# Kernel optimization log

Measured on AMD Instinct MI355X. Metric: run time of the kernel, lower is better.

Reference implementation:

```python
import jax, jax.numpy as jnp
import numpy as np

N_NODES = 2048
UNITS = 64
IN_DIM = 64
K_DIFF = 2  # max_diffusion_step


def _rw_norm_t(adj):
    # random-walk normalize D^{-1}(A+I), then transpose (as in forward())
    a = adj + jnp.eye(adj.shape[0], dtype=adj.dtype)
    d = jnp.sum(a, axis=1)
    d_inv = jnp.where(d > 0, 1.0 / jnp.where(d > 0, d, 1.0), 0.0)
    return (d_inv[:, None] * a).T


def _gconv(x_cat, adj_t, W, b):
    # x_cat: (B, N, F). Chebyshev-like diffusion: x0, A x0, 2 A x1 - x0, ...
    x0 = x_cat
    xs = [x0]
    x1 = jnp.einsum('nm,bmf->bnf', adj_t, x0)
    xs.append(x1)
    for _ in range(2, K_DIFF + 1):
        x2 = 2.0 * jnp.einsum('nm,bmf->bnf', adj_t, x1) - x0
        xs.append(x2)
        x0, x1 = x1, x2
    x = jnp.stack(xs, axis=-1)  # (B, N, F, K+1) -> matches torch permute(3,1,2,0)
    B, N, F, K = x.shape
    x = x.reshape(B * N, F * K)
    out = x @ W + b
    return out.reshape(B, N, -1)


def setup_inputs() -> dict:
    key = jax.random.key(0)
    ks = jax.random.split(key, 6)
    B = 64
    inputs = jax.random.normal(ks[0], (B, N_NODES * IN_DIM), dtype=jnp.float32)
    hx = jax.random.normal(ks[1], (B, N_NODES * UNITS), dtype=jnp.float32)
    adj = jax.random.uniform(ks[2], (N_NODES, N_NODES), dtype=jnp.float32)
    in_sz = IN_DIM + UNITS
    nm = K_DIFF + 1
    scale = float(np.sqrt(2.0 / (in_sz * nm + 2 * UNITS)))  # xavier-ish
    W_ru = jax.random.normal(ks[3], (in_sz * nm, 2 * UNITS), dtype=jnp.float32) * scale
    b_ru = jnp.ones((2 * UNITS,), dtype=jnp.float32)  # bias_start=1.0
    W_c = jax.random.normal(ks[4], (in_sz * nm, UNITS), dtype=jnp.float32) * scale
    b_c = jnp.zeros((UNITS,), dtype=jnp.float32)
    return {"inputs": inputs, "hx": hx, "adj": adj,
            "W_ru": W_ru, "b_ru": b_ru, "W_c": W_c, "b_c": b_c}


def reference(inputs, hx, adj, W_ru, b_ru, W_c, b_c):
    B = inputs.shape[0]
    x = inputs.reshape(B, N_NODES, IN_DIM)
    h = hx.reshape(B, N_NODES, UNITS)
    adj_t = _rw_norm_t(adj)
    # r/u gates via graph conv + sigmoid
    ru = jax.nn.sigmoid(_gconv(jnp.concatenate([x, h], axis=-1), adj_t, W_ru, b_ru))
    r, u = ru[..., :UNITS], ru[..., UNITS:]
    # candidate state
    c = jnp.tanh(_gconv(jnp.concatenate([x, r * h], axis=-1), adj_t, W_c, b_c))
    new_state = u * h + (1.0 - u) * c
    return new_state.reshape(B, N_NODES * UNITS)
```

## Files before the change

kernel.cpp:

```cpp
#include <hip/hip_runtime.h>
#include <math.h>

typedef __attribute__((ext_vector_type(8))) short short8;
typedef __attribute__((ext_vector_type(4))) float float4v;
typedef __attribute__((ext_vector_type(16))) float float16v;
typedef __attribute__((ext_vector_type(4))) unsigned short ushort4v;
typedef unsigned short u16;
typedef unsigned int u32;

#define NB 64
#define NN 2048
#define FD 128
#define UD 64
#define KT 384


__device__ __forceinline__ u16 f2bf(float f) {
    unsigned int u = __float_as_uint(f);
    u += 0x7fffu + ((u >> 16) & 1u);
    return (u16)(u >> 16);
}
__device__ __forceinline__ float bf2f(u16 s) {
    return __uint_as_float(((unsigned int)s) << 16);
}
__device__ __forceinline__ float sigmoidf_(float x) {
    return 1.0f / (1.0f + expf(-x));
}
__device__ __forceinline__ void gl2lds16(const u16* g, u16* l) {
    __builtin_amdgcn_global_load_lds((const __attribute__((address_space(1))) unsigned int*)g,
                                     (__attribute__((address_space(3))) unsigned int*)l,
                                     16, 0, 0);
}

__global__ void k_prep(const float* __restrict__ adj, float* __restrict__ d_inv,
                       const float* __restrict__ W_ru, u16* __restrict__ Wru,
                       const float* __restrict__ W_c,  u16* __restrict__ Wc,
                       const float* __restrict__ x, const float* __restrict__ h,
                       u16* __restrict__ X0f, u16* __restrict__ X0m) {
    __shared__ u16 T[128 * 136];
    int bid = blockIdx.x;
    int t = threadIdx.x;
    if (bid < 2048) {
        int m = bid;
        const float4v* row = (const float4v*)(adj + (size_t)m * NN);
        float s = 0.f;
        for (int i = t; i < NN / 4; i += 256) {
            float4v v = row[i];
            s += v.x + v.y + v.z + v.w;
        }
        float* red = (float*)T;
        for (int off = 32; off; off >>= 1) s += __shfl_down(s, off, 64);
        if ((t & 63) == 0) red[t >> 6] = s;
        __syncthreads();
        if (t == 0) {
            float tt = red[0] + red[1] + red[2] + red[3] + 1.0f;
            d_inv[m] = 1.0f / tt;
        }
        return;
    }
    if (bid < 2336) {
        const float* W; u16* Wt; int OD, idx;
        if (bid < 2240) { W = W_ru; Wt = Wru; OD = FD; idx = (bid - 2048) * 256 + t; }
        else            { W = W_c;  Wt = Wc;  OD = UD; idx = (bid - 2240) * 256 + t; }
        if (idx >= KT * OD) return;
        int o  = idx % OD;
        int kp = idx / OD;
        int kd = kp >> 7, f = kp & 127;
        float v;
        if (kd == 0)      v = W[(size_t)(f * 3 + 0) * OD + o] - W[(size_t)(f * 3 + 2) * OD + o];
        else if (kd == 1) v = W[(size_t)(f * 3 + 1) * OD + o];
        else              v = 2.0f * W[(size_t)(f * 3 + 2) * OD + o];
        size_t dst = ((size_t)(o >> 5) * 12 + (kp >> 5)) * 1024 + (((kp >> 3) & 3) * 32 + (o & 31)) * 8 + (kp & 7);
        Wt[dst] = f2bf(v);
        return;
    }
    int rb = bid - 2336;
    int m0 = (rb & 15) * 128;
    int b  = rb >> 4;
    const float* srcs[2] = { x + (size_t)b * (NN * 64), h + (size_t)b * (NN * 64) };
    for (int s = 0; s < 2; ++s) {
        const float* src = srcs[s];
        for (int p = 0; p < 8; ++p) {
            int idx = t + 256 * p;
            int mi = idx >> 4;
            int f4 = idx & 15;
            float4v v = *(const float4v*)(src + (size_t)(m0 + mi) * 64 + f4 * 4);
            float vv[4] = {v.x, v.y, v.z, v.w};
#pragma unroll
            for (int j = 0; j < 4; ++j)
                T[(s * 64 + f4 * 4 + j) * 136 + mi] = f2bf(vv[j]);
        }
    }
    __syncthreads();
#pragma unroll
    for (int p = 0; p < 8; ++p) {
        int S = t + 256 * p;
        int fgl = S >> 9, kgl = (S >> 7) & 3, s = S & 127;
        int c = s >> 5, r = s & 31;
        short8 v = *(const short8*)(T + (fgl * 32 + r) * 136 + kgl * 32 + c * 8);
        *(short8*)(X0f + ((size_t)(b * 4 + fgl) * 64 + (m0 >> 5) + kgl) * 1024 + s * 8) = v;
    }
#pragma unroll
    for (int p = 0; p < 8; ++p) {
        int S = t + 256 * p;
        int fc = S >> 7;
        int mi = S & 127;
        short8 v;
#pragma unroll
        for (int e = 0; e < 8; ++e) v[e] = (short)T[(fc * 8 + e) * 136 + mi];
        size_t dst = ((size_t)(b * 64 + (m0 >> 5) + (mi >> 5)) * 4 + (fc >> 2)) * 1024
                     + ((fc & 3) * 32 + (mi & 31)) * 8;
        *(short8*)(X0m + dst) = v;
    }
}

__global__ void k_adjT(const float* __restrict__ adj, const float* __restrict__ d_inv,
                       u16* __restrict__ adjT) {
    __shared__ u16 T[64 * 72];
    int m0 = blockIdx.x * 64;
    int n0 = blockIdx.y * 64;
    int t = threadIdx.x;
    for (int p = 0; p < 4; ++p) {
        int idx = t + 256 * p;
        int i  = idx >> 4;
        int n4 = idx & 15;
        int m = m0 + i;
        float4v v = *(const float4v*)(adj + (size_t)m * NN + n0 + n4 * 4);
        float di = d_inv[m];
        float vv[4] = {v.x, v.y, v.z, v.w};
#pragma unroll
        for (int j = 0; j < 4; ++j) {
            int n = n0 + n4 * 4 + j;
            float a = vv[j] + ((m == n) ? 1.0f : 0.0f);
            T[(n4 * 4 + j) * 72 + i] = f2bf(a * di);
        }
    }
    __syncthreads();
#pragma unroll
    for (int p = 0; p < 2; ++p) {
        int S = t + 256 * p;
        int rgl = S >> 8, kgl = (S >> 7) & 1, s = S & 127;
        int c = s >> 5, r = s & 31;
        short8 v = *(const short8*)(T + (rgl * 32 + r) * 72 + kgl * 32 + c * 8);
        *(short8*)(adjT + ((size_t)((n0 >> 5) + rgl) * 64 + (m0 >> 5) + kgl) * 1024 + s * 8) = v;
    }
}

template<int HAS_F>
__global__ __launch_bounds__(512, 2)
void k_gemm256(const u16* __restrict__ Ap, const u16* __restrict__ Bc,
               u16* __restrict__ outF, u16* __restrict__ outM) {
    __shared__ __align__(16) u16 SM[81920];
    int bid = blockIdx.x;
    int wxcd = bid >> 3;
    int cb = (bid & 7) * 4 + (wxcd & 3);
    int nb = wxcd >> 2;
    int n0 = nb * 256, c0 = cb * 256;
    int t = threadIdx.x;
    int wave = t >> 6, lane = t & 63;
    int wx = wave >> 2;
    int wy = wave & 3;
    int ln = lane & 31, hi = lane >> 5;

    const u16* gA[2];
    const u16* gB[2];
    int la[2], lb[2];
#pragma unroll
    for (int i = 0; i < 2; ++i) {
        int idx = i * 512 + t;
        int p = idx >> 7, s = idx & 127;
        gA[i] = Bc + ((size_t)((c0 >> 5) + p) * 64) * 1024 + s * 8;
        gB[i] = Ap + ((size_t)((n0 >> 5) + p) * 64) * 1024 + s * 8;
        la[i] = idx * 8;
        lb[i] = 8192 + idx * 8;
    }

    float16v acc[4][2];
#pragma unroll
    for (int mt = 0; mt < 4; ++mt)
#pragma unroll
        for (int nt = 0; nt < 2; ++nt)
#pragma unroll
            for (int e = 0; e < 16; ++e) acc[mt][nt][e] = 0.f;

#pragma unroll
    for (int tt = 0; tt < 4; ++tt) {
#pragma unroll
        for (int i = 0; i < 2; ++i) gl2lds16(gA[i] + tt * 1024, SM + tt * 16384 + la[i]);
#pragma unroll
        for (int i = 0; i < 2; ++i) gl2lds16(gB[i] + tt * 1024, SM + tt * 16384 + lb[i]);
    }
    asm volatile("s_waitcnt vmcnt(12)" ::: "memory");
    __builtin_amdgcn_s_barrier();
    __builtin_amdgcn_sched_barrier(0);

    int rdA = wx * 4096 + lane * 8;
    int rdB = 8192 + wy * 2048 + lane * 8;

    int cur = 0;
    for (int kt = 0; kt < 64; ++kt) {
        u16* buf = SM + cur * 16384;
        int stg = cur + 4; if (stg >= 5) stg -= 5;
        u16* sbuf = SM + stg * 16384;
        size_t ko = (size_t)(kt + 4) * 1024;

        short8 fa0[4], fb0[2], fa1[4], fb1[2];
#pragma unroll
        for (int mt = 0; mt < 4; ++mt) fa0[mt] = *(const short8*)(buf + rdA + mt * 1024);
#pragma unroll
        for (int nt = 0; nt < 2; ++nt) fb0[nt] = *(const short8*)(buf + rdB + nt * 1024);
        if (kt < 60) {
#pragma unroll
            for (int i = 0; i < 2; ++i) gl2lds16(gA[i] + ko, sbuf + la[i]);
        }
#pragma unroll
        for (int mt = 0; mt < 4; ++mt) fa1[mt] = *(const short8*)(buf + rdA + mt * 1024 + 512);

        __builtin_amdgcn_s_setprio(1);
#pragma unroll
        for (int mt = 0; mt < 4; ++mt)
#pragma unroll
            for (int nt = 0; nt < 2; ++nt)
                acc[mt][nt] = __builtin_amdgcn_mfma_f32_32x32x16_bf16(fa0[mt], fb0[nt], acc[mt][nt], 0, 0, 0);
        __builtin_amdgcn_s_setprio(0);

#pragma unroll
        for (int nt = 0; nt < 2; ++nt) fb1[nt] = *(const short8*)(buf + rdB + nt * 1024 + 512);
        if (kt < 60) {
#pragma unroll
            for (int i = 0; i < 2; ++i) gl2lds16(gB[i] + ko, sbuf + lb[i]);
        }

        __builtin_amdgcn_s_setprio(1);
#pragma unroll
        for (int mt = 0; mt < 4; ++mt)
#pragma unroll
            for (int nt = 0; nt < 2; ++nt)
                acc[mt][nt] = __builtin_amdgcn_mfma_f32_32x32x16_bf16(fa1[mt], fb1[nt], acc[mt][nt], 0, 0, 0);
        __builtin_amdgcn_s_setprio(0);

        if (kt < 60)       asm volatile("s_waitcnt vmcnt(12)" ::: "memory");
        else if (kt == 60) asm volatile("s_waitcnt vmcnt(8)"  ::: "memory");
        else if (kt == 61) asm volatile("s_waitcnt vmcnt(4)"  ::: "memory");
        else if (kt == 62) asm volatile("s_waitcnt vmcnt(0)"  ::: "memory");
        if (kt < 63) {
            __builtin_amdgcn_s_barrier();
            __builtin_amdgcn_sched_barrier(0);
        }
        cur = (cur + 1 == 5) ? 0 : cur + 1;
    }

    int batch0 = cb * 2 + wx;
#pragma unroll
    for (int mt = 0; mt < 4; ++mt) {
#pragma unroll
        for (int nt = 0; nt < 2; ++nt) {
            int mg = (n0 >> 5) + wy * 2 + nt;
            size_t pbase = ((size_t)(batch0 * 64 + mg) * 4 + mt) * 1024;
#pragma unroll
            for (int eq = 0; eq < 4; ++eq) {
                ushort4v pk;
#pragma unroll
                for (int r = 0; r < 4; ++r) pk[r] = f2bf(acc[mt][nt][eq * 4 + r]);
                *(ushort4v*)(outM + pbase + (eq * 32 + ln) * 8 + 4 * hi) = pk;
            }
        }
    }

    if (HAS_F) {
#pragma unroll
        for (int p = 0; p < 2; ++p) {
            __syncthreads();
            if ((wy >> 1) == p) {
#pragma unroll
                for (int mt = 0; mt < 4; ++mt)
#pragma unroll
                    for (int nt = 0; nt < 2; ++nt)
#pragma unroll
                        for (int e = 0; e < 16; ++e) {
                            int cl = wx * 128 + mt * 32 + 4 * hi + 8 * (e >> 2) + (e & 3);
                            int nl = (wy & 1) * 64 + nt * 32 + ln;
                            SM[cl * 136 + nl] = f2bf(acc[mt][nt][e]);
                        }
            }
            __syncthreads();
#pragma unroll
            for (int j = 0; j < 8; ++j) {
                int S = t + 512 * j;
                int col = S >> 4, nd8 = S & 15;
                short8 v = *(const short8*)(SM + col * 136 + nd8 * 8);
                int gn = n0 + p * 128 + nd8 * 8;
                size_t dst = ((size_t)((c0 >> 5) + (col >> 5)) * 64 + (gn >> 5)) * 1024
                             + (size_t)((((gn >> 3) & 3) * 32 + (col & 31))) * 8;
                *(short8*)(outF + dst) = v;
            }
        }
    }
}

template<int FG>
__global__ __launch_bounds__(256, 4)
void k_gemm(const u16* __restrict__ A, const u16* __restrict__ Bc,
            u16* __restrict__ outF, u16* __restrict__ outM, int cBlocks) {
    __shared__ u16 SM[16384];
    u16* A0 = SM;            u16* A1 = SM + 4096;
    u16* B0 = SM + 8192;     u16* B1 = SM + 12288;

    int id = blockIdx.x + cBlocks * blockIdx.y;
    int band = cBlocks >> 3;
    int g = id & 7, s = id >> 3;
    int cb = g * band + (s % band);
    int nb = s / band;
    int c0 = cb * 128;
    int n0 = nb * 128;

    int t = threadIdx.x;
    int wave = t >> 6, lane = t & 63;
    int wy = wave & 1, wx = wave >> 1;
    int ln = lane & 31, hi = lane >> 5;
    int l16 = lane * 8;

    const u16* gaP[2];
    const u16* gbP[2];
#pragma unroll
    for (int i = 0; i < 2; ++i) {
        int T = t + 256 * i;
        gaP[i] = A  + ((size_t)((n0 >> 5) + (T >> 7)) * 64) * 1024 + (size_t)(T & 127) * 8;
        gbP[i] = Bc + ((size_t)((c0 >> 5) + (T >> 7)) * 64) * 1024 + (size_t)(T & 127) * 8;
    }

    float16v acc[2][2];
#pragma unroll
    for (int i = 0; i < 2; ++i)
#pragma unroll
        for (int j = 0; j < 2; ++j)
#pragma unroll
            for (int e = 0; e < 16; ++e) acc[i][j][e] = 0.f;

#pragma unroll
    for (int i = 0; i < 2; ++i) { gl2lds16(gaP[i], A0 + (t + 256 * i) * 8); gl2lds16(gbP[i], B0 + (t + 256 * i) * 8); }

#pragma unroll 2
    for (int it = 0; it < 64; ++it) {
        u16* Ac = (it & 1) ? A1 : A0;
        u16* Bs = (it & 1) ? B1 : B0;
        __syncthreads();
        if (it + 1 < 64) {
            int ko = (it + 1) * 1024;
            u16* An = (it & 1) ? A0 : A1;
            u16* Bn = (it & 1) ? B0 : B1;
#pragma unroll
            for (int i = 0; i < 2; ++i) { gl2lds16(gaP[i] + ko, An + (t + 256 * i) * 8); gl2lds16(gbP[i] + ko, Bn + (t + 256 * i) * 8); }
        }
        short8 fa[2][2], fb[2][2];
#pragma unroll
        for (int ks = 0; ks < 2; ++ks) {
#pragma unroll
            for (int mt = 0; mt < 2; ++mt)
                fa[ks][mt] = *(const short8*)(Bs + ((wx * 2 + mt) * 2 + ks) * 512 + l16);
#pragma unroll
            for (int nt = 0; nt < 2; ++nt)
                fb[ks][nt] = *(const short8*)(Ac + ((wy * 2 + nt) * 2 + ks) * 512 + l16);
        }
#pragma unroll
        for (int ks = 0; ks < 2; ++ks)
#pragma unroll
            for (int mt = 0; mt < 2; ++mt)
#pragma unroll
                for (int nt = 0; nt < 2; ++nt)
                    acc[mt][nt] = __builtin_amdgcn_mfma_f32_32x32x16_bf16(fa[ks][mt], fb[ks][nt], acc[mt][nt], 0, 0, 0);
    }

#pragma unroll
    for (int mt = 0; mt < 2; ++mt) {
#pragma unroll
        for (int nt = 0; nt < 2; ++nt) {
            int mg = (n0 >> 5) + wy * 2 + nt;
            int batch = (FG == 4) ? cb : (2 * cb + wx);
            int fg = (FG == 4) ? (wx * 2 + mt) : mt;
            size_t pbase = ((size_t)(batch * 64 + mg) * FG + fg) * 1024;
#pragma unroll
            for (int eq = 0; eq < 4; ++eq) {
                ushort4v pk;
#pragma unroll
                for (int r = 0; r < 4; ++r) pk[r] = f2bf(acc[mt][nt][eq * 4 + r]);
                *(ushort4v*)(outM + pbase + (eq * 32 + ln) * 8 + 4 * hi) = pk;
            }
        }
    }

    if (outF) {
        __syncthreads();
#pragma unroll
        for (int p = 0; p < 2; ++p) {
            if (p) __syncthreads();
            if (wx == p) {
#pragma unroll
                for (int mt = 0; mt < 2; ++mt)
#pragma unroll
                    for (int nt = 0; nt < 2; ++nt)
#pragma unroll
                        for (int e = 0; e < 16; ++e) {
                            int cl = mt * 32 + 4 * hi + 8 * (e >> 2) + (e & 3);
                            int nl = wy * 64 + nt * 32 + ln;
                            SM[cl * 136 + nl] = f2bf(acc[mt][nt][e]);
                        }
            }
            __syncthreads();
#pragma unroll
            for (int pp = 0; pp < 4; ++pp) {
                int S = t + 256 * pp;
                int rgl = S >> 9, kgl = (S >> 7) & 3, sl = S & 127;
                int c = sl >> 5, r = sl & 31;
                short8 v = *(const short8*)(SM + (rgl * 32 + r) * 136 + kgl * 32 + c * 8);
                size_t gaddr = ((size_t)((c0 >> 5) + p * 2 + rgl) * 64 + (n0 >> 5) + kgl) * 1024 + sl * 8;
                *(short8*)(outF + gaddr) = v;
            }
        }
    }
}

__global__ __launch_bounds__(256, 3)
void k_proj_ru(const u16* __restrict__ X0m, const u16* __restrict__ X1m, const u16* __restrict__ Ym,
               const u16* __restrict__ Wp, const float* __restrict__ bias, const float* __restrict__ hx,
               u16* __restrict__ RH0f, u16* __restrict__ RH0m, u16* __restrict__ Ut) {
    __shared__ u16 SM[24576];
    int mb = blockIdx.x, b = blockIdx.y;
    int m0 = mb * 128, mg0 = mb * 4;
    int t = threadIdx.x, wave = t >> 6, lane = t & 63;
    int wx = wave & 1, wyy = wave >> 1;
    int ln = lane & 31, hi = lane >> 5;
    const u16* Xs[3] = {X0m, X1m, Ym};
    int p0 = t >> 7, s0 = t & 127;

    float16v acc[2][2];
#pragma unroll
    for (int i = 0; i < 2; ++i)
#pragma unroll
        for (int j = 0; j < 2; ++j)
#pragma unroll
            for (int e = 0; e < 16; ++e) acc[i][j][e] = 0.f;

#define STAGE_RU(Q, XD, WD) { \
    const u16* xb_ = Xs[(Q) >> 2]; \
    gl2lds16(xb_ + ((size_t)((b * 64 + mg0 + p0) * 4 + ((Q) & 3))) * 1024 + s0 * 8, (XD) + t * 8); \
    gl2lds16(xb_ + ((size_t)((b * 64 + mg0 + p0 + 2) * 4 + ((Q) & 3))) * 1024 + s0 * 8, (XD) + (t + 256) * 8); \
    gl2lds16(Wp + ((size_t)(p0 * 12 + (Q))) * 1024 + s0 * 8, (WD) + t * 8); \
    gl2lds16(Wp + ((size_t)((p0 + 2) * 12 + (Q))) * 1024 + s0 * 8, (WD) + (t + 256) * 8); }

    STAGE_RU(0, SM,        SM + 12288);
    STAGE_RU(1, SM + 4096, SM + 16384);
    asm volatile("s_waitcnt vmcnt(4)" ::: "memory");
    __builtin_amdgcn_s_barrier();
    __builtin_amdgcn_sched_barrier(0);

    int q0 = 0, q1 = 1, q2 = 2;
    for (int kq = 0; kq < 12; ++kq) {
        u16* Xc = SM + q0 * 4096;
        u16* Wc = SM + 12288 + q0 * 4096;
        if (kq + 2 < 12) STAGE_RU(kq + 2, SM + q2 * 4096, SM + 12288 + q2 * 4096);
        short8 fa[2][2], fb[2][2];
#pragma unroll
        for (int ks = 0; ks < 2; ++ks) {
#pragma unroll
            for (int mt = 0; mt < 2; ++mt)
                fa[ks][mt] = *(const short8*)(Xc + ((wx * 2 + mt) * 2 + ks) * 512 + lane * 8);
#pragma unroll
            for (int nt = 0; nt < 2; ++nt)
                fb[ks][nt] = *(const short8*)(Wc + ((wyy * 2 + nt) * 2 + ks) * 512 + lane * 8);
        }
        __builtin_amdgcn_s_setprio(1);
#pragma unroll
        for (int ks = 0; ks < 2; ++ks)
#pragma unroll
            for (int mt = 0; mt < 2; ++mt)
#pragma unroll
                for (int nt = 0; nt < 2; ++nt)
                    acc[mt][nt] = __builtin_amdgcn_mfma_f32_32x32x16_bf16(fa[ks][mt], fb[ks][nt], acc[mt][nt], 0, 0, 0);
        __builtin_amdgcn_s_setprio(0);
        if (kq < 10)       asm volatile("s_waitcnt vmcnt(4)" ::: "memory");
        else if (kq == 10) asm volatile("s_waitcnt vmcnt(0)" ::: "memory");
        if (kq < 11) {
            __builtin_amdgcn_s_barrier();
            __builtin_amdgcn_sched_barrier(0);
        }
        int tq = q0; q0 = q1; q1 = q2; q2 = tq;
    }
#undef STAGE_RU

    __syncthreads();
    if (wyy == 0) {
#pragma unroll
        for (int mt = 0; mt < 2; ++mt)
#pragma unroll
            for (int nt = 0; nt < 2; ++nt) {
                int o = nt * 32 + ln;
                float bo = bias[o];
                u16 vals[16];
#pragma unroll
                for (int e = 0; e < 16; ++e) {
                    int ml = wx * 64 + mt * 32 + 4 * hi + 8 * (e >> 2) + (e & 3);
                    float sg = sigmoidf_(acc[mt][nt][e] + bo);
                    float hh = hx[((size_t)b * NN + m0 + ml) * 64 + o];
                    vals[e] = f2bf(sg * hh);
                    SM[ml * 76 + o] = vals[e];
                }
#pragma unroll
                for (int eq = 0; eq < 4; ++eq) {
                    ushort4v pk;
#pragma unroll
                    for (int r = 0; r < 4; ++r) pk[r] = vals[eq * 4 + r];
                    size_t addr = ((size_t)(b * 2 + nt) * 64 + mg0 + wx * 2 + mt) * 1024 + (eq * 32 + ln) * 8 + 4 * hi;
                    *(ushort4v*)(RH0f + addr) = pk;
                }
            }
    } else {
#pragma unroll
        for (int mt = 0; mt < 2; ++mt)
#pragma unroll
            for (int nt = 0; nt < 2; ++nt) {
                int og = nt * 32 + ln;
                float bo = bias[64 + og];
#pragma unroll
                for (int e = 0; e < 16; ++e) {
                    int ml = wx * 64 + mt * 32 + 4 * hi + 8 * (e >> 2) + (e & 3);
                    Ut[((size_t)b * NN + m0 + ml) * 64 + og] = f2bf(sigmoidf_(acc[mt][nt][e] + bo));
                }
            }
    }
    __syncthreads();
#pragma unroll
    for (int j = 0; j < 4; ++j) {
        int C = t + 256 * j;
        int p = C >> 7, sl = C & 127;
        int mgl = p >> 1, ug = p & 1;
        int cq = sl >> 5, r = sl & 31;
        short8 v = *(const short8*)(SM + (mgl * 32 + r) * 76 + ug * 32 + cq * 8);
        *(short8*)(RH0m + ((size_t)((b * 64 + mg0 + mgl) * 2 + ug)) * 1024 + sl * 8) = v;
    }
}

__global__ __launch_bounds__(256, 4)
void k_proj_c(const u16* __restrict__ X0m, const u16* __restrict__ X1m, const u16* __restrict__ Ym,
              const u16* __restrict__ RH0m, const u16* __restrict__ RH1m, const u16* __restrict__ Zm,
              const u16* __restrict__ Wp, const float* __restrict__ bias,
              const float* __restrict__ hx, const u16* __restrict__ Ut,
              float* __restrict__ out) {
    __shared__ u16 SM[18432];
    int mb = blockIdx.x, b = blockIdx.y;
    int m0 = mb * 128, mg0 = mb * 4;
    int t = threadIdx.x, wave = t >> 6, lane = t & 63;
    int wx = wave & 1, wyy = wave >> 1;
    int ln = lane & 31, hi = lane >> 5;
    const u16* Xs[3] = {X0m, X1m, Ym};
    const u16* Rs[3] = {RH0m, RH1m, Zm};
    int p0 = t >> 7, s0 = t & 127;

    float16v acc[2];
#pragma unroll
    for (int i = 0; i < 2; ++i)
#pragma unroll
        for (int e = 0; e < 16; ++e) acc[i][e] = 0.f;

#define STAGE_C(Q, XD, WD) { \
    int fb2_ = ((Q) & 3) * 32; \
    const u16* mat_; size_t pb0_, pb1_; \
    if (fb2_ < 64) { \
        mat_ = Xs[(Q) >> 2]; \
        pb0_ = ((size_t)((b * 64 + mg0 + p0) * 4 + (fb2_ >> 5))) * 1024; \
        pb1_ = ((size_t)((b * 64 + mg0 + p0 + 2) * 4 + (fb2_ >> 5))) * 1024; \
    } else { \
        mat_ = Rs[(Q) >> 2]; \
        pb0_ = ((size_t)((b * 64 + mg0 + p0) * 2 + ((fb2_ >> 5) - 2))) * 1024; \
        pb1_ = ((size_t)((b * 64 + mg0 + p0 + 2) * 2 + ((fb2_ >> 5) - 2))) * 1024; \
    } \
    gl2lds16(mat_ + pb0_ + s0 * 8, (XD) + t * 8); \
    gl2lds16(mat_ + pb1_ + s0 * 8, (XD) + (t + 256) * 8); \
    gl2lds16(Wp + ((size_t)(p0 * 12 + (Q))) * 1024 + s0 * 8, (WD) + t * 8); }

    STAGE_C(0, SM,        SM + 12288);
    STAGE_C(1, SM + 4096, SM + 14336);
    asm volatile("s_waitcnt vmcnt(3)" ::: "memory");
    __builtin_amdgcn_s_barrier();
    __builtin_amdgcn_sched_barrier(0);

    int q0 = 0, q1 = 1, q2 = 2;
    for (int kq = 0; kq < 12; ++kq) {
        u16* Xc = SM + q0 * 4096;
        u16* Wc = SM + 12288 + q0 * 2048;
        if (kq + 2 < 12) STAGE_C(kq + 2, SM + q2 * 4096, SM + 12288 + q2 * 2048);
        short8 fa[2][2], fbg[2];
#pragma unroll
        for (int ks = 0; ks < 2; ++ks) {
#pragma unroll
            for (int mt = 0; mt < 2; ++mt)
                fa[ks][mt] = *(const short8*)(Xc + ((wx * 2 + mt) * 2 + ks) * 512 + lane * 8);
            fbg[ks] = *(const short8*)(Wc + (wyy * 2 + ks) * 512 + lane * 8);
        }
        __builtin_amdgcn_s_setprio(1);
#pragma unroll
        for (int ks = 0; ks < 2; ++ks)
#pragma unroll
            for (int mt = 0; mt < 2; ++mt)
                acc[mt] = __builtin_amdgcn_mfma_f32_32x32x16_bf16(fa[ks][mt], fbg[ks], acc[mt], 0, 0, 0);
        __builtin_amdgcn_s_setprio(0);
        if (kq < 10)       asm volatile("s_waitcnt vmcnt(3)" ::: "memory");
        else if (kq == 10) asm volatile("s_waitcnt vmcnt(0)" ::: "memory");
        if (kq < 11) {
            __builtin_amdgcn_s_barrier();
            __builtin_amdgcn_sched_barrier(0);
        }
        int tq = q0; q0 = q1; q1 = q2; q2 = tq;
    }
#undef STAGE_C

    int o = wyy * 32 + ln;
    float bo = bias[o];
#pragma unroll
    for (int mt = 0; mt < 2; ++mt)
#pragma unroll
        for (int e = 0; e < 16; ++e) {
            int ml = wx * 64 + mt * 32 + 4 * hi + 8 * (e >> 2) + (e & 3);
            size_t idx = ((size_t)b * NN + m0 + ml) * 64 + o;
            float c = tanhf(acc[mt][e] + bo);
            float u = bf2f(Ut[idx]);
            float hh = hx[idx];
            out[idx] = u * hh + (1.0f - u) * c;
        }
}

extern "C" void kernel_launch(void* const* d_in, const int* in_sizes, int n_in,
                              void* d_out, int out_size, void* d_ws, size_t ws_size,
                              hipStream_t stream) {
    const float* x    = (const float*)d_in[0];
    const float* hx   = (const float*)d_in[1];
    const float* adj  = (const float*)d_in[2];
    const float* W_ru = (const float*)d_in[3];
    const float* b_ru = (const float*)d_in[4];
    const float* W_c  = (const float*)d_in[5];
    const float* b_c  = (const float*)d_in[6];
    float* out = (float*)d_out;

    char* ws = (char*)d_ws;
    size_t off = 0;
    auto alloc = [&](size_t bytes) -> void* {
        void* p = ws + off;
        off += (bytes + 255) & ~(size_t)255;
        return p;
    };
    float* d_inv = (float*)alloc((size_t)NN * 4);
    u16* adjT = (u16*)alloc((size_t)NN * NN * 2);
    u16* Wru  = (u16*)alloc((size_t)FD * KT * 2);
    u16* Wc   = (u16*)alloc((size_t)UD * KT * 2);
    u16* X0f = (u16*)alloc((size_t)NB * FD * NN * 2);
    u16* X1f = (u16*)alloc((size_t)NB * FD * NN * 2);
    u16* X0m = (u16*)alloc((size_t)NB * FD * NN * 2);
    u16* X1m = (u16*)alloc((size_t)NB * FD * NN * 2);
    u16* Ym  = (u16*)alloc((size_t)NB * FD * NN * 2);
    u16* RH0m = (u16*)alloc((size_t)NB * UD * NN * 2);
    u16* RH1m = (u16*)alloc((size_t)NB * UD * NN * 2);
    u16* Zm   = (u16*)alloc((size_t)NB * UD * NN * 2);
    u16* Ut   = (u16*)alloc((size_t)NB * UD * NN * 2);
    u16* RH0f = X0f;
    u16* RH1f = X1f;

    k_prep<<<dim3(3360), dim3(256), 0, stream>>>(adj, d_inv, W_ru, Wru, W_c, Wc, x, hx, X0f, X0m);
    k_adjT<<<dim3(32, 32), dim3(256), 0, stream>>>(adj, d_inv, adjT);
    k_gemm256<1><<<dim3(256), dim3(512), 0, stream>>>(adjT, X0f, X1f, X1m);
    k_gemm256<0><<<dim3(256), dim3(512), 0, stream>>>(adjT, X1f, nullptr, Ym);
    k_proj_ru<<<dim3(16, NB), dim3(256), 0, stream>>>(X0m, X1m, Ym, Wru, b_ru, hx, RH0f, RH0m, Ut);
    k_gemm<2><<<dim3(32, 16), dim3(256), 0, stream>>>(adjT, RH0f, RH1f, RH1m, 32);
    k_gemm<2><<<dim3(32, 16), dim3(256), 0, stream>>>(adjT, RH1f, nullptr, Zm, 32);
    k_proj_c<<<dim3(16, NB), dim3(256), 0, stream>>>(X0m, X1m, Ym, RH0m, RH1m, Zm, Wc, b_c, hx, Ut, out);
}
```

Measured before the change: 425.5 us.

## Replace RH diffusion GEMM with 256-node tile, 5-stage LDS pipeline kernel

Replaces the 128x128-tile double-buffered GEMM used for the two r*h diffusion steps with a 512-thread kernel that computes 256-node by 128-column tiles. Operands stream through a 5-deep LDS ring with explicit vmcnt waits and one barrier per k-step, and MFMA sections are raised in priority with s_setprio. The output transpose is done in a single pass. The aim is to hide global load latency and reuse each adjT tile across more columns, at the cost of a large LDS footprint that allows only one block per CU.

```diff
diff --git a/kernel.cpp b/kernel.cpp
--- a/kernel.cpp
+++ b/kernel.cpp
@@ -298,87 +298,111 @@
     }
 }
 
-template<int FG>
-__global__ __launch_bounds__(256, 4)
-void k_gemm(const u16* __restrict__ A, const u16* __restrict__ Bc,
-            u16* __restrict__ outF, u16* __restrict__ outM, int cBlocks) {
-    __shared__ u16 SM[16384];
-    u16* A0 = SM;            u16* A1 = SM + 4096;
-    u16* B0 = SM + 8192;     u16* B1 = SM + 12288;
-
-    int id = blockIdx.x + cBlocks * blockIdx.y;
-    int band = cBlocks >> 3;
-    int g = id & 7, s = id >> 3;
-    int cb = g * band + (s % band);
-    int nb = s / band;
-    int c0 = cb * 128;
-    int n0 = nb * 128;
-
+template<int HAS_F>
+__global__ __launch_bounds__(512, 1)
+void k_gemmRH(const u16* __restrict__ Ap, const u16* __restrict__ Bc,
+              u16* __restrict__ outF, u16* __restrict__ outM) {
+    __shared__ __align__(16) u16 SM[61440];
+    int bid = blockIdx.x;
+    int wxcd = bid >> 3;
+    int cb = (bid & 7) * 4 + (wxcd & 3);
+    int nb = wxcd >> 2;
+    int n0 = nb * 256, c0 = cb * 128;
     int t = threadIdx.x;
     int wave = t >> 6, lane = t & 63;
-    int wy = wave & 1, wx = wave >> 1;
+    int wx = wave >> 2;
+    int wy = wave & 3;
     int ln = lane & 31, hi = lane >> 5;
-    int l16 = lane * 8;
-
-    const u16* gaP[2];
-    const u16* gbP[2];
+
+    const u16* gA = Bc + ((size_t)((c0 >> 5) + (t >> 7)) * 64) * 1024 + (size_t)(t & 127) * 8;
+    int la = t * 8;
+    const u16* gB[2];
+    int lb[2];
 #pragma unroll
     for (int i = 0; i < 2; ++i) {
-        int T = t + 256 * i;
-        gaP[i] = A  + ((size_t)((n0 >> 5) + (T >> 7)) * 64) * 1024 + (size_t)(T & 127) * 8;
-        gbP[i] = Bc + ((size_t)((c0 >> 5) + (T >> 7)) * 64) * 1024 + (size_t)(T & 127) * 8;
+        int idx = i * 512 + t;
+        gB[i] = Ap + ((size_t)((n0 >> 5) + (idx >> 7)) * 64) * 1024 + (size_t)(idx & 127) * 8;
+        lb[i] = 4096 + idx * 8;
     }
 
     float16v acc[2][2];
 #pragma unroll
-    for (int i = 0; i < 2; ++i)
-#pragma unroll
-        for (int j = 0; j < 2; ++j)
-#pragma unroll
-            for (int e = 0; e < 16; ++e) acc[i][j][e] = 0.f;
-
-#pragma unroll
-    for (int i = 0; i < 2; ++i) { gl2lds16(gaP[i], A0 + (t + 256 * i) * 8); gl2lds16(gbP[i], B0 + (t + 256 * i) * 8); }
-
-#pragma unroll 2
-    for (int it = 0; it < 64; ++it) {
-        u16* Ac = (it & 1) ? A1 : A0;
-        u16* Bs = (it & 1) ? B1 : B0;
-        __syncthreads();
-        if (it + 1 < 64) {
-            int ko = (it + 1) * 1024;
-            u16* An = (it & 1) ? A0 : A1;
-            u16* Bn = (it & 1) ? B0 : B1;
-#pragma unroll
-            for (int i = 0; i < 2; ++i) { gl2lds16(gaP[i] + ko, An + (t + 256 * i) * 8); gl2lds16(gbP[i] + ko, Bn + (t + 256 * i) * 8); }
-        }
-        short8 fa[2][2], fb[2][2];
-#pragma unroll
-        for (int ks = 0; ks < 2; ++ks) {
-#pragma unroll
-            for (int mt = 0; mt < 2; ++mt)
-                fa[ks][mt] = *(const short8*)(Bs + ((wx * 2 + mt) * 2 + ks) * 512 + l16);
+    for (int mt = 0; mt < 2; ++mt)
+#pragma unroll
+        for (int nt = 0; nt < 2; ++nt)
+#pragma unroll
+            for (int e = 0; e < 16; ++e) acc[mt][nt][e] = 0.f;
+
+#pragma unroll
+    for (int tt = 0; tt < 4; ++tt) {
+        gl2lds16(gA + tt * 1024, SM + tt * 12288 + la);
+#pragma unroll
+        for (int i = 0; i < 2; ++i) gl2lds16(gB[i] + tt * 1024, SM + tt * 12288 + lb[i]);
+    }
+    asm volatile("s_waitcnt vmcnt(9)" ::: "memory");
+    __builtin_amdgcn_s_barrier();
+    __builtin_amdgcn_sched_barrier(0);
+
+    int rdA = wx * 2048 + lane * 8;
+    int rdB = 4096 + wy * 2048 + lane * 8;
+
+    int cur = 0;
+    for (int kt = 0; kt < 64; ++kt) {
+        u16* buf = SM + cur * 12288;
+        int stg = cur + 4; if (stg >= 5) stg -= 5;
+        u16* sbuf = SM + stg * 12288;
+        size_t ko = (size_t)(kt + 4) * 1024;
+
+        short8 fa0[2], fb0[2], fa1[2], fb1[2];
+#pragma unroll
+        for (int mt = 0; mt < 2; ++mt) fa0[mt] = *(const short8*)(buf + rdA + mt * 1024);
+#pragma unroll
+        for (int nt = 0; nt < 2; ++nt) fb0[nt] = *(const short8*)(buf + rdB + nt * 1024);
+        if (kt < 60) gl2lds16(gA + ko, sbuf + la);
+#pragma unroll
+        for (int mt = 0; mt < 2; ++mt) fa1[mt] = *(const short8*)(buf + rdA + mt * 1024 + 512);
+
+        __builtin_amdgcn_s_setprio(1);
+#pragma unroll
+        for (int mt = 0; mt < 2; ++mt)
 #pragma unroll
             for (int nt = 0; nt < 2; ++nt)
-                fb[ks][nt] = *(const short8*)(Ac + ((wy * 2 + nt) * 2 + ks) * 512 + l16);
-        }
-#pragma unroll
-        for (int ks = 0; ks < 2; ++ks)
-#pragma unroll
-            for (int mt = 0; mt < 2; ++mt)
-#pragma unroll
-                for (int nt = 0; nt < 2; ++nt)
-                    acc[mt][nt] = __builtin_amdgcn_mfma_f32_32x32x16_bf16(fa[ks][mt], fb[ks][nt], acc[mt][nt], 0, 0, 0);
-    }
-
+                acc[mt][nt] = __builtin_amdgcn_mfma_f32_32x32x16_bf16(fa0[mt], fb0[nt], acc[mt][nt], 0, 0, 0);
+        __builtin_amdgcn_s_setprio(0);
+
+#pragma unroll
+        for (int nt = 0; nt < 2; ++nt) fb1[nt] = *(const short8*)(buf + rdB + nt * 1024 + 512);
+        if (kt < 60) {
+#pragma unroll
+            for (int i = 0; i < 2; ++i) gl2lds16(gB[i] + ko, sbuf + lb[i]);
+        }
+
+        __builtin_amdgcn_s_setprio(1);
+#pragma unroll
+        for (int mt = 0; mt < 2; ++mt)
+#pragma unroll
+            for (int nt = 0; nt < 2; ++nt)
+                acc[mt][nt] = __builtin_amdgcn_mfma_f32_32x32x16_bf16(fa1[mt], fb1[nt], acc[mt][nt], 0, 0, 0);
+        __builtin_amdgcn_s_setprio(0);
+
+        if (kt < 60)       asm volatile("s_waitcnt vmcnt(9)" ::: "memory");
+        else if (kt == 60) asm volatile("s_waitcnt vmcnt(6)" ::: "memory");
+        else if (kt == 61) asm volatile("s_waitcnt vmcnt(3)" ::: "memory");
+        else if (kt == 62) asm volatile("s_waitcnt vmcnt(0)" ::: "memory");
+        if (kt < 63) {
+            __builtin_amdgcn_s_barrier();
+            __builtin_amdgcn_sched_barrier(0);
+        }
+        cur = (cur + 1 == 5) ? 0 : cur + 1;
+    }
+
+    int batch0 = cb * 2 + wx;
 #pragma unroll
     for (int mt = 0; mt < 2; ++mt) {
 #pragma unroll
         for (int nt = 0; nt < 2; ++nt) {
             int mg = (n0 >> 5) + wy * 2 + nt;
-            int batch = (FG == 4) ? cb : (2 * cb + wx);
-            int fg = (FG == 4) ? (wx * 2 + mt) : mt;
-            size_t pbase = ((size_t)(batch * 64 + mg) * FG + fg) * 1024;
+            size_t pbase = ((size_t)(batch0 * 64 + mg) * 2 + mt) * 1024;
 #pragma unroll
             for (int eq = 0; eq < 4; ++eq) {
                 ushort4v pk;
@@ -389,33 +413,27 @@
         }
     }
 
-    if (outF) {
+    if (HAS_F) {
         __syncthreads();
 #pragma unroll
-        for (int p = 0; p < 2; ++p) {
-            if (p) __syncthreads();
-            if (wx == p) {
-#pragma unroll
-                for (int mt = 0; mt < 2; ++mt)
-#pragma unroll
-                    for (int nt = 0; nt < 2; ++nt)
-#pragma unroll
-                        for (int e = 0; e < 16; ++e) {
-                            int cl = mt * 32 + 4 * hi + 8 * (e >> 2) + (e & 3);
-                            int nl = wy * 64 + nt * 32 + ln;
-                            SM[cl * 136 + nl] = f2bf(acc[mt][nt][e]);
-                        }
-            }
-            __syncthreads();
-#pragma unroll
-            for (int pp = 0; pp < 4; ++pp) {
-                int S = t + 256 * pp;
-                int rgl = S >> 9, kgl = (S >> 7) & 3, sl = S & 127;
-                int c = sl >> 5, r = sl & 31;
-                short8 v = *(const short8*)(SM + (rgl * 32 + r) * 136 + kgl * 32 + c * 8);
-                size_t gaddr = ((size_t)((c0 >> 5) + p * 2 + rgl) * 64 + (n0 >> 5) + kgl) * 1024 + sl * 8;
-                *(short8*)(outF + gaddr) = v;
-            }
+        for (int mt = 0; mt < 2; ++mt)
+#pragma unroll
+            for (int nt = 0; nt < 2; ++nt)
+#pragma unroll
+                for (int e = 0; e < 16; ++e) {
+                    int col = wx * 64 + mt * 32 + 4 * hi + 8 * (e >> 2) + (e & 3);
+                    int node = wy * 64 + nt * 32 + ln;
+                    SM[col * 264 + node] = f2bf(acc[mt][nt][e]);
+                }
+        __syncthreads();
+#pragma unroll
+        for (int j = 0; j < 8; ++j) {
+            int S = t + 512 * j;
+            int col = S >> 5, nd8 = S & 31;
+            short8 v = *(const short8*)(SM + col * 264 + nd8 * 8);
+            size_t dst = ((size_t)((c0 >> 5) + (col >> 5)) * 64 + (n0 >> 5) + (nd8 >> 2)) * 1024
+                         + (size_t)((nd8 & 3) * 32 + (col & 31)) * 8;
+            *(short8*)(outF + dst) = v;
         }
     }
 }
@@ -669,7 +687,7 @@
     k_gemm256<1><<<dim3(256), dim3(512), 0, stream>>>(adjT, X0f, X1f, X1m);
     k_gemm256<0><<<dim3(256), dim3(512), 0, stream>>>(adjT, X1f, nullptr, Ym);
     k_proj_ru<<<dim3(16, NB), dim3(256), 0, stream>>>(X0m, X1m, Ym, Wru, b_ru, hx, RH0f, RH0m, Ut);
-    k_gemm<2><<<dim3(32, 16), dim3(256), 0, stream>>>(adjT, RH0f, RH1f, RH1m, 32);
-    k_gemm<2><<<dim3(32, 16), dim3(256), 0, stream>>>(adjT, RH1f, nullptr, Zm, 32);
+    k_gemmRH<1><<<dim3(256), dim3(512), 0, stream>>>(adjT, RH0f, RH1f, RH1m);
+    k_gemmRH<0><<<dim3(256), dim3(512), 0, stream>>>(adjT, RH1f, nullptr, Zm);
     k_proj_c<<<dim3(16, NB), dim3(256), 0, stream>>>(X0m, X1m, Ym, RH0m, RH1m, Zm, Wc, b_c, hx, Ut, out);
 }
```

Result: slower. 454.4 us (+6.8%).

## Deepen k_gemm LDS pipeline to four stages with explicit vmcnt waits

Applied to the files above, without the earlier changes.

Replaces the double-buffered LDS staging in k_gemm with a four-slot ring buffer that prefetches three K-tiles ahead. Synchronization moves from __syncthreads to explicit s_waitcnt vmcnt counts plus a raw s_barrier, with s_setprio raised around the MFMA block. The goal is to hide global-to-LDS load latency better. In exchange, LDS use doubles and launch bounds drop to 2 blocks per CU, which lowers occupancy.

```diff
diff --git a/kernel.cpp b/kernel.cpp
--- a/kernel.cpp
+++ b/kernel.cpp
@@ -299,12 +299,10 @@
 }
 
 template<int FG>
-__global__ __launch_bounds__(256, 4)
+__global__ __launch_bounds__(256, 2)
 void k_gemm(const u16* __restrict__ A, const u16* __restrict__ Bc,
             u16* __restrict__ outF, u16* __restrict__ outM, int cBlocks) {
-    __shared__ u16 SM[16384];
-    u16* A0 = SM;            u16* A1 = SM + 4096;
-    u16* B0 = SM + 8192;     u16* B1 = SM + 12288;
+    __shared__ __align__(16) u16 SM[32768];
 
     int id = blockIdx.x + cBlocks * blockIdx.y;
     int band = cBlocks >> 3;
@@ -338,30 +336,41 @@
             for (int e = 0; e < 16; ++e) acc[i][j][e] = 0.f;
 
 #pragma unroll
-    for (int i = 0; i < 2; ++i) { gl2lds16(gaP[i], A0 + (t + 256 * i) * 8); gl2lds16(gbP[i], B0 + (t + 256 * i) * 8); }
-
-#pragma unroll 2
+    for (int tt = 0; tt < 3; ++tt) {
+#pragma unroll
+        for (int i = 0; i < 2; ++i) {
+            gl2lds16(gaP[i] + tt * 1024, SM + tt * 8192 + (t + 256 * i) * 8);
+            gl2lds16(gbP[i] + tt * 1024, SM + tt * 8192 + 4096 + (t + 256 * i) * 8);
+        }
+    }
+    asm volatile("s_waitcnt vmcnt(8)" ::: "memory");
+    __builtin_amdgcn_s_barrier();
+    __builtin_amdgcn_sched_barrier(0);
+
+    int cur = 0;
     for (int it = 0; it < 64; ++it) {
-        u16* Ac = (it & 1) ? A1 : A0;
-        u16* Bs = (it & 1) ? B1 : B0;
-        __syncthreads();
-        if (it + 1 < 64) {
-            int ko = (it + 1) * 1024;
-            u16* An = (it & 1) ? A0 : A1;
-            u16* Bn = (it & 1) ? B0 : B1;
-#pragma unroll
-            for (int i = 0; i < 2; ++i) { gl2lds16(gaP[i] + ko, An + (t + 256 * i) * 8); gl2lds16(gbP[i] + ko, Bn + (t + 256 * i) * 8); }
+        u16* buf  = SM + cur * 8192;
+        u16* sbuf = SM + ((cur + 3) & 3) * 8192;
+        size_t ko = (size_t)(it + 3) * 1024;
+
+        if (it < 61) {
+#pragma unroll
+            for (int i = 0; i < 2; ++i) {
+                gl2lds16(gaP[i] + ko, sbuf + (t + 256 * i) * 8);
+                gl2lds16(gbP[i] + ko, sbuf + 4096 + (t + 256 * i) * 8);
+            }
         }
         short8 fa[2][2], fb[2][2];
 #pragma unroll
         for (int ks = 0; ks < 2; ++ks) {
 #pragma unroll
             for (int mt = 0; mt < 2; ++mt)
-                fa[ks][mt] = *(const short8*)(Bs + ((wx * 2 + mt) * 2 + ks) * 512 + l16);
+                fa[ks][mt] = *(const short8*)(buf + 4096 + ((wx * 2 + mt) * 2 + ks) * 512 + l16);
 #pragma unroll
             for (int nt = 0; nt < 2; ++nt)
-                fb[ks][nt] = *(const short8*)(Ac + ((wy * 2 + nt) * 2 + ks) * 512 + l16);
-        }
+                fb[ks][nt] = *(const short8*)(buf + ((wy * 2 + nt) * 2 + ks) * 512 + l16);
+        }
+        __builtin_amdgcn_s_setprio(1);
 #pragma unroll
         for (int ks = 0; ks < 2; ++ks)
 #pragma unroll
@@ -369,6 +378,16 @@
 #pragma unroll
                 for (int nt = 0; nt < 2; ++nt)
                     acc[mt][nt] = __builtin_amdgcn_mfma_f32_32x32x16_bf16(fa[ks][mt], fb[ks][nt], acc[mt][nt], 0, 0, 0);
+        __builtin_amdgcn_s_setprio(0);
+
+        if (it < 61)       asm volatile("s_waitcnt vmcnt(8)" ::: "memory");
+        else if (it == 61) asm volatile("s_waitcnt vmcnt(4)" ::: "memory");
+        else if (it == 62) asm volatile("s_waitcnt vmcnt(0)" ::: "memory");
+        if (it < 63) {
+            __builtin_amdgcn_s_barrier();
+            __builtin_amdgcn_sched_barrier(0);
+        }
+        cur = (cur + 1) & 3;
     }
 
 #pragma unroll
```

Result: no change. 425.8 us (+0.1%).
